# Kernel optimization log

Measured on AMD Instinct MI355X. Metric: run time of the kernel, lower is better.

## Reference

```python
import jax, jax.numpy as jnp
import numpy as np

N = 100000
IN_DIM = 512
HID = 5
HEADS1 = 5
NUM_CLASSES = 3
NEG_SLOPE = 0.2


def _gat_conv(x, src, dst, W, a_src, a_dst, b, heads, out_ch, concat):
    """PyG-style GATConv (eval mode, self-loops already included in src/dst)."""
    n = x.shape[0]
    h = (x @ W).reshape(n, heads, out_ch)                      # [N,H,C]
    alpha_src = jnp.einsum('nhc,hc->nh', h, a_src)             # [N,H]
    alpha_dst = jnp.einsum('nhc,hc->nh', h, a_dst)             # [N,H]
    e = jax.nn.leaky_relu(alpha_src[src] + alpha_dst[dst], NEG_SLOPE)  # [E,H]
    # segment softmax over edges grouped by destination node
    m = jax.ops.segment_max(e, dst, num_segments=n)            # [N,H]
    ex = jnp.exp(e - m[dst])
    denom = jax.ops.segment_sum(ex, dst, num_segments=n)       # [N,H]
    alpha = ex / denom[dst]                                    # [E,H]
    out = jax.ops.segment_sum(alpha[:, :, None] * h[src], dst, num_segments=n)  # [N,H,C]
    out = out.reshape(n, heads * out_ch) if concat else out.mean(axis=1)
    return out + b


def setup_inputs() -> dict:
    key = jax.random.key(0)
    ks = jax.random.split(key, 10)
    E = 3200000
    x = jax.random.normal(ks[0], (N, IN_DIM), dtype=jnp.float32)
    edge_index = jax.random.randint(ks[1], (2, E), 0, N, dtype=jnp.int64)
    s1 = 1.0 / np.sqrt(IN_DIM)
    s2 = 1.0 / np.sqrt(HID * HEADS1)
    return {
        'x': x,
        'edge_index': edge_index,
        'W1': jax.random.normal(ks[2], (IN_DIM, HEADS1 * HID), dtype=jnp.float32) * s1,
        'att_src1': jax.random.normal(ks[3], (HEADS1, HID), dtype=jnp.float32),
        'att_dst1': jax.random.normal(ks[4], (HEADS1, HID), dtype=jnp.float32),
        'bias1': jnp.zeros((HEADS1 * HID,), dtype=jnp.float32),
        'W2': jax.random.normal(ks[5], (HEADS1 * HID, NUM_CLASSES), dtype=jnp.float32) * s2,
        'att_src2': jax.random.normal(ks[6], (1, NUM_CLASSES), dtype=jnp.float32),
        'att_dst2': jax.random.normal(ks[7], (1, NUM_CLASSES), dtype=jnp.float32),
        'bias2': jnp.zeros((NUM_CLASSES,), dtype=jnp.float32),
    }


def reference(x, edge_index, W1, att_src1, att_dst1, bias1, W2, att_src2, att_dst2, bias2):
    # add self loops (PyG GATConv default)
    loops = jnp.arange(N, dtype=edge_index.dtype)
    src = jnp.concatenate([edge_index[0], loops])
    dst = jnp.concatenate([edge_index[1], loops])
    h = _gat_conv(x, src, dst, W1, att_src1, att_dst1, bias1, HEADS1, HID, True)
    h = jax.nn.elu(h)
    out = _gat_conv(h, src, dst, W2, att_src2, att_dst2, bias2, 1, NUM_CLASSES, False)
    return jax.nn.log_sigmoid(out)
```

## Files before the change

kernel.cpp:

```cpp
#include <hip/hip_runtime.h>
#include <math.h>

#define N_NODES 100000
#define IN_DIM  512
#define HID     5
#define HEADS   5
#define C1      25
#define NC      3
#define NEG     0.2f
#define NPB     64
#define BSH     7
#define NBUCK   ((N_NODES + 127) >> BSH)
#define NDIG    1024
#define NBH2    512
#define HTH2    256
#define BCAP    6144

typedef float f32x4 __attribute__((ext_vector_type(4)));

struct __attribute__((packed, aligned(4))) H6 { _Float16 a; _Float16 h[5]; };

__device__ __forceinline__ float lrelu(float v) { return v >= 0.f ? v : NEG * v; }

__device__ __forceinline__ void fma4(float acc[C1], f32x4 xv, const float* w) {
#pragma unroll
    for (int j = 0; j < C1; ++j)
        acc[j] = __builtin_fmaf(xv.w, w[3 * C1 + j],
                 __builtin_fmaf(xv.z, w[2 * C1 + j],
                 __builtin_fmaf(xv.y, w[C1 + j],
                 __builtin_fmaf(xv.x, w[j], acc[j]))));
}

__global__ void __launch_bounds__(256)
k_gemm_hist(const float* __restrict__ x, const float* __restrict__ W1,
            const float* __restrict__ as1, const float* __restrict__ ad1,
            const int* __restrict__ ei, int E, int TOT, int NG,
            _Float16* __restrict__ h1p, float* __restrict__ adst,
            int* __restrict__ hist) {
    __shared__ float red[3][64][C1];
    int b = blockIdx.x;
    int tid = threadIdx.x;
    if (b >= NG) {
        int* lh = (int*)red;
        int hb = b - NG;
        for (int i = tid; i < NDIG; i += HTH2) lh[i] = 0;
        __syncthreads();
        int chunk = (TOT + NBH2 - 1) / NBH2;
        int e0 = hb * chunk, e1 = min(e0 + chunk, TOT);
        for (int e = e0 + tid; e < e1; e += HTH2) {
            int d = (e < E) ? ei[E + e] : e - E;
            atomicAdd(&lh[d >> BSH], 1);
        }
        __syncthreads();
        for (int i = tid; i < NDIG; i += HTH2) hist[hb * NDIG + i] = lh[i];
        return;
    }
    int c = __builtin_amdgcn_readfirstlane(tid >> 6);
    int l = tid & 63;
    int n = b * 64 + l;
    int nc = n < N_NODES ? n : N_NODES - 1;
    const f32x4* xr = (const f32x4*)(x + (size_t)nc * IN_DIM) + c * 32;
    const float* Wb = W1 + (size_t)c * 128 * C1;
    float acc[C1];
#pragma unroll
    for (int j = 0; j < C1; ++j) acc[j] = 0.f;
    for (int L = 0; L < 8; ++L) {
        f32x4 xv[4];
#pragma unroll
        for (int q = 0; q < 4; ++q) xv[q] = xr[L * 4 + q];
#pragma unroll
        for (int q = 0; q < 4; ++q)
            fma4(acc, xv[q], Wb + (size_t)(L * 4 + q) * 4 * C1);
    }
    if (c > 0) {
#pragma unroll
        for (int j = 0; j < C1; ++j) red[c - 1][l][j] = acc[j];
    }
    __syncthreads();
    if (c == 0 && n < N_NODES) {
#pragma unroll
        for (int j = 0; j < C1; ++j)
            acc[j] += red[0][l][j] + red[1][l][j] + red[2][l][j];
        _Float16 hb16[32];
#pragma unroll
        for (int h = 0; h < HEADS; ++h) {
            float s = 0.f, d = 0.f;
#pragma unroll
            for (int cc = 0; cc < HID; ++cc) {
                s += acc[h * HID + cc] * as1[h * HID + cc];
                d += acc[h * HID + cc] * ad1[h * HID + cc];
                hb16[6 * h + 1 + cc] = (_Float16)acc[h * HID + cc];
            }
            hb16[6 * h] = (_Float16)s;
            adst[n * HEADS + h] = d;
        }
        hb16[30] = (_Float16)0.f; hb16[31] = (_Float16)0.f;
        float4* h4 = (float4*)(h1p + (size_t)n * 32);
        const float4* src = (const float4*)hb16;
#pragma unroll
        for (int q = 0; q < 4; ++q) h4[q] = src[q];
    }
}

__global__ void __launch_bounds__(NBH2)
k_colscan(int* __restrict__ hist, int* __restrict__ bcnt) {
    __shared__ int sh[NBH2];
    int d = blockIdx.x, t = threadIdx.x;
    int v = hist[t * NDIG + d];
    sh[t] = v;
    __syncthreads();
    for (int ofs = 1; ofs < NBH2; ofs <<= 1) {
        int u = (t >= ofs) ? sh[t - ofs] : 0;
        __syncthreads();
        sh[t] += u;
        __syncthreads();
    }
    hist[t * NDIG + d] = sh[t] - v;
    if (t == NBH2 - 1) bcnt[d] = sh[t];
}

__global__ void __launch_bounds__(NDIG)
k_boff(const int* __restrict__ bcnt, int* __restrict__ boff) {
    __shared__ int sh[NDIG];
    int t = threadIdx.x;
    int v = bcnt[t];
    sh[t] = v;
    __syncthreads();
    for (int ofs = 1; ofs < NDIG; ofs <<= 1) {
        int u = (t >= ofs) ? sh[t - ofs] : 0;
        __syncthreads();
        sh[t] += u;
        __syncthreads();
    }
    boff[t] = sh[t] - v;
}

__global__ void __launch_bounds__(HTH2)
k_write(const int* __restrict__ ei, int E, int TOT, const int* __restrict__ hist,
        const int* __restrict__ boff, int* __restrict__ pk) {
    __shared__ int lbase[NDIG];
    __shared__ int lcur[NDIG];
    int b = blockIdx.x, tid = threadIdx.x;
    for (int i = tid; i < NDIG; i += HTH2) {
        lbase[i] = boff[i] + hist[b * NDIG + i];
        lcur[i] = 0;
    }
    __syncthreads();
    int chunk = (TOT + NBH2 - 1) / NBH2;
    int e0 = b * chunk, e1 = min(e0 + chunk, TOT);
    for (int e = e0 + tid; e < e1; e += HTH2) {
        int s, d;
        if (e < E) { s = ei[e]; d = ei[E + e]; } else { s = d = e - E; }
        int dg = d >> BSH;
        int r = atomicAdd(&lcur[dg], 1);
        pk[lbase[dg] + r] = s | ((d & 127) << 17);
    }
}

__global__ void __launch_bounds__(512)
k_bgroup(const int* __restrict__ boff, const int* __restrict__ bcnt,
         const int* __restrict__ pk, int* __restrict__ off, int* __restrict__ deg,
         int* __restrict__ ssrc) {
    __shared__ int stage[BCAP];
    __shared__ int cnt[128], pref[128], lcur[128];
    int b = blockIdx.x, tid = threadIdx.x;
    int n0 = b << BSH;
    if (tid < 128) cnt[tid] = 0;
    __syncthreads();
    int r0 = boff[b], total = bcnt[b];
    for (int idx = tid; idx < total; idx += 512) {
        int v = pk[r0 + idx];
        if (idx < BCAP) stage[idx] = v;
        atomicAdd(&cnt[(v >> 17) & 127], 1);
    }
    __syncthreads();
    if (tid < 128) pref[tid] = cnt[tid];
    __syncthreads();
    for (int ofs = 1; ofs < 128; ofs <<= 1) {
        int u = 0;
        if (tid < 128 && tid >= ofs) u = pref[tid - ofs];
        __syncthreads();
        if (tid < 128) pref[tid] += u;
        __syncthreads();
    }
    if (tid < 128) {
        int n = n0 + tid;
        if (n < N_NODES) {
            off[n] = r0 + pref[tid] - cnt[tid];
            deg[n] = cnt[tid];
        }
        lcur[tid] = 0;
    }
    __syncthreads();
    for (int idx = tid; idx < total; idx += 512) {
        int v = (idx < BCAP) ? stage[idx] : pk[r0 + idx];
        int dl = (v >> 17) & 127;
        int r = atomicAdd(&lcur[dl], 1);
        ssrc[r0 + pref[dl] - cnt[dl] + r] = v & 0x1FFFF;
    }
}

__global__ void __launch_bounds__(NPB * HEADS)
k_layer1(const int* __restrict__ off, const int* __restrict__ deg, const int* __restrict__ ssrc,
         const _Float16* __restrict__ h1p, const float* __restrict__ adst,
         const float* __restrict__ b1, const float* __restrict__ W2,
         const float* __restrict__ as2, const float* __restrict__ ad2,
         float4* __restrict__ n2, float* __restrict__ a2d) {
    __shared__ float sh[NPB * C1];
    int tid = threadIdx.x;
    int ln = tid / HEADS, h = tid % HEADS;
    int n = blockIdx.x * NPB + ln;
    if (n < N_NODES) {
        int st = off[n], cnt = deg[n];
        float adn = adst[n * HEADS + h];
        float den = 0.f;
        float num[HID] = {0.f, 0.f, 0.f, 0.f, 0.f};
        const H6* hp = (const H6*)(h1p) + h;
        for (int i = 0; i < cnt; ++i) {
            int s = ssrc[st + i];
            H6 hv = *(const H6*)((const _Float16*)hp + (size_t)s * 32 - (size_t)0);
            float p = __expf(lrelu((float)hv.a + adn));
            den += p;
#pragma unroll
            for (int c = 0; c < HID; ++c) num[c] = __builtin_fmaf(p, (float)hv.h[c], num[c]);
        }
        float inv = 1.f / den;
#pragma unroll
        for (int c = 0; c < HID; ++c) {
            float v = num[c] * inv + b1[h * HID + c];
            sh[ln * C1 + h * HID + c] = v > 0.f ? v : expm1f(v);
        }
    }
    __syncthreads();
    if (tid < NPB) {
        int nn = blockIdx.x * NPB + tid;
        if (nn < N_NODES) {
            float gg[NC] = {0.f, 0.f, 0.f};
#pragma unroll
            for (int j = 0; j < C1; ++j) {
                float hv = sh[tid * C1 + j];
#pragma unroll
                for (int c = 0; c < NC; ++c) gg[c] += hv * W2[j * NC + c];
            }
            float ssv = 0.f, ddv = 0.f;
#pragma unroll
            for (int c = 0; c < NC; ++c) { ssv += gg[c] * as2[c]; ddv += gg[c] * ad2[c]; }
            n2[nn] = make_float4(ssv, gg[0], gg[1], gg[2]);
            a2d[nn] = ddv;
        }
    }
}

__global__ void k_layer2(const int* __restrict__ off, const int* __restrict__ deg,
                         const int* __restrict__ ssrc, const float4* __restrict__ n2,
                         const float* __restrict__ a2d, const float* __restrict__ b2,
                         float* __restrict__ out) {
    int n = blockIdx.x * blockDim.x + threadIdx.x;
    if (n >= N_NODES) return;
    int st = off[n], cnt = deg[n];
    float adn = a2d[n];
    float den = 0.f, num0 = 0.f, num1 = 0.f, num2 = 0.f;
    for (int i = 0; i < cnt; ++i) {
        int s = ssrc[st + i];
        float4 gv = n2[s];
        float p = __expf(lrelu(gv.x + adn));
        den += p;
        num0 = __builtin_fmaf(p, gv.y, num0);
        num1 = __builtin_fmaf(p, gv.z, num1);
        num2 = __builtin_fmaf(p, gv.w, num2);
    }
    float inv = 1.f / den;
    float vv[NC] = {num0 * inv + b2[0], num1 * inv + b2[1], num2 * inv + b2[2]};
#pragma unroll
    for (int c = 0; c < NC; ++c) {
        float v = vv[c];
        out[n * NC + c] = (v >= 0.f) ? -log1pf(__expf(-v)) : v - log1pf(__expf(v));
    }
}

extern "C" void kernel_launch(void* const* d_in, const int* in_sizes, int n_in,
                              void* d_out, int out_size, void* d_ws, size_t ws_size,
                              hipStream_t stream) {
    const float* x   = (const float*)d_in[0];
    const int*   ei  = (const int*)d_in[1];
    const float* W1  = (const float*)d_in[2];
    const float* as1 = (const float*)d_in[3];
    const float* ad1 = (const float*)d_in[4];
    const float* b1  = (const float*)d_in[5];
    const float* W2  = (const float*)d_in[6];
    const float* as2 = (const float*)d_in[7];
    const float* ad2 = (const float*)d_in[8];
    const float* b2  = (const float*)d_in[9];
    float* out = (float*)d_out;
    int E = in_sizes[1] / 2;
    int TOT = E + N_NODES;

    int*   iws = (int*)d_ws;
    float* fws = (float*)d_ws;
    int* hist = iws;
    int* bcnt = iws + 524288;
    int* boff = iws + 525312;
    int* off  = iws + 526336;
    int* deg  = iws + 626336;
    int* pk   = iws + 726336;
    int* ssrc = pk + TOT;
    size_t fbase = 726336 + 2 * (size_t)TOT;
    _Float16* h1p = (_Float16*)(fws + fbase);
    float*  adst = fws + fbase + 1600000;
    float4* n2   = (float4*)(fws + fbase + 2100000);
    float*  a2d  = fws + fbase + 2500000;

    dim3 blk(256);
    int NB1 = (N_NODES + 255) / 256;
    int NG  = (N_NODES + 63) / 64;
    k_gemm_hist<<<dim3(NG + NBH2), dim3(256), 0, stream>>>(
        x, W1, as1, ad1, ei, E, TOT, NG, h1p, adst, hist);
    k_colscan<<<dim3(NDIG), dim3(NBH2), 0, stream>>>(hist, bcnt);
    k_boff<<<dim3(1), dim3(NDIG), 0, stream>>>(bcnt, boff);
    k_write<<<dim3(NBH2), dim3(HTH2), 0, stream>>>(ei, E, TOT, hist, boff, pk);
    k_bgroup<<<dim3(NBUCK), dim3(512), 0, stream>>>(boff, bcnt, pk, off, deg, ssrc);
    k_layer1<<<dim3((N_NODES + NPB - 1) / NPB), dim3(NPB * HEADS), 0, stream>>>(
        off, deg, ssrc, h1p, adst, b1, W2, as2, ad2, n2, a2d);
    k_layer2<<<dim3(NB1), blk, 0, stream>>>(off, deg, ssrc, n2, a2d, b2, out);
}
```

Baseline: 285.7 us.

## Stage x rows through padded LDS for coalesced loads in layer-1 GEMM

Previously each lane read its own node's 512-float x row, so a wavefront touched 64 widely strided rows per load. Now each group of 4 threads cooperatively loads one row in 128-column chunks into padded LDS (stride 130), register-prefetching the next chunk while computing from LDS. Each wave then reads its K-slice from shared memory. This makes global reads contiguous at the cost of extra LDS traffic and barriers per chunk.

Result: slower. 314.0 us (+9.9%).

```diff
diff --git a/kernel.cpp b/kernel.cpp
--- a/kernel.cpp
+++ b/kernel.cpp
@@ -15,6 +15,7 @@
 #define NBH2    512
 #define HTH2    256
 #define BCAP    6144
+#define LSTR    130
 
 typedef float f32x4 __attribute__((ext_vector_type(4)));
 
@@ -37,11 +38,11 @@
             const int* __restrict__ ei, int E, int TOT, int NG,
             _Float16* __restrict__ h1p, float* __restrict__ adst,
             int* __restrict__ hist) {
-    __shared__ float red[3][64][C1];
+    __shared__ float lds[64 * LSTR];
     int b = blockIdx.x;
     int tid = threadIdx.x;
     if (b >= NG) {
-        int* lh = (int*)red;
+        int* lh = (int*)lds;
         int hb = b - NG;
         for (int i = tid; i < NDIG; i += HTH2) lh[i] = 0;
         __syncthreads();
@@ -55,32 +56,57 @@
         for (int i = tid; i < NDIG; i += HTH2) hist[hb * NDIG + i] = lh[i];
         return;
     }
-    int c = __builtin_amdgcn_readfirstlane(tid >> 6);
+    int w = __builtin_amdgcn_readfirstlane(tid >> 6);
     int l = tid & 63;
-    int n = b * 64 + l;
-    int nc = n < N_NODES ? n : N_NODES - 1;
-    const f32x4* xr = (const f32x4*)(x + (size_t)nc * IN_DIM) + c * 32;
-    const float* Wb = W1 + (size_t)c * 128 * C1;
+    int nbase = b * 64;
+    int n = nbase + l;
+    int rsub = tid >> 2;
+    int j4 = tid & 3;
+    int nst = nbase + rsub;
+    int nstc = nst < N_NODES ? nst : N_NODES - 1;
+    const float* xrow = x + (size_t)nstc * IN_DIM;
+
     float acc[C1];
 #pragma unroll
     for (int j = 0; j < C1; ++j) acc[j] = 0.f;
-    for (int L = 0; L < 8; ++L) {
-        f32x4 xv[4];
-#pragma unroll
-        for (int q = 0; q < 4; ++q) xv[q] = xr[L * 4 + q];
-#pragma unroll
-        for (int q = 0; q < 4; ++q)
-            fma4(acc, xv[q], Wb + (size_t)(L * 4 + q) * 4 * C1);
-    }
-    if (c > 0) {
-#pragma unroll
-        for (int j = 0; j < C1; ++j) red[c - 1][l][j] = acc[j];
-    }
-    __syncthreads();
-    if (c == 0 && n < N_NODES) {
+
+    f32x4 st[8];
+#pragma unroll
+    for (int q = 0; q < 8; ++q)
+        st[q] = *(const f32x4*)(xrow + (j4 + 4 * q) * 4);
+
+    for (int ck = 0; ck < 4; ++ck) {
+        __syncthreads();
+#pragma unroll
+        for (int q = 0; q < 8; ++q) {
+            float* p = &lds[rsub * LSTR + (j4 + 4 * q) * 4];
+            p[0] = st[q].x; p[1] = st[q].y; p[2] = st[q].z; p[3] = st[q].w;
+        }
+        __syncthreads();
+        if (ck < 3) {
+#pragma unroll
+            for (int q = 0; q < 8; ++q)
+                st[q] = *(const f32x4*)(xrow + (ck + 1) * 128 + (j4 + 4 * q) * 4);
+        }
+        const float* Wb = W1 + (size_t)(ck * 128 + w * 32) * C1;
+#pragma unroll
+        for (int kk = 0; kk < 8; ++kk) {
+            f32x4 xv = *(const f32x4*)(&lds[l * LSTR + w * 32 + kk * 4]);
+            fma4(acc, xv, Wb + (size_t)kk * 4 * C1);
+        }
+    }
+    float* red = lds;
+    __syncthreads();
+    if (w > 0) {
+#pragma unroll
+        for (int j = 0; j < C1; ++j) red[((w - 1) * 64 + l) * 26 + j] = acc[j];
+    }
+    __syncthreads();
+    if (w == 0 && n < N_NODES) {
 #pragma unroll
         for (int j = 0; j < C1; ++j)
-            acc[j] += red[0][l][j] + red[1][l][j] + red[2][l][j];
+            acc[j] += red[(0 * 64 + l) * 26 + j] + red[(1 * 64 + l) * 26 + j]
+                    + red[(2 * 64 + l) * 26 + j];
         _Float16 hb16[32];
 #pragma unroll
         for (int h = 0; h < HEADS; ++h) {
@@ -218,7 +244,7 @@
         const H6* hp = (const H6*)(h1p) + h;
         for (int i = 0; i < cnt; ++i) {
             int s = ssrc[st + i];
-            H6 hv = *(const H6*)((const _Float16*)hp + (size_t)s * 32 - (size_t)0);
+            H6 hv = *(const H6*)((const _Float16*)hp + (size_t)s * 32);
             float p = __expf(lrelu((float)hv.a + adn));
             den += p;
 #pragma unroll
```
